# Kernel optimization log

Hardware: AMD Instinct MI355X
Metric: run time of the kernel (lower is better)

Reference implementation:

```python
import jax, jax.numpy as jnp
import numpy as np

C64 = jnp.complex64


def _ry(t):  # scalar angle -> [2,2] complex
    c = jnp.cos(t / 2).astype(C64)
    s = jnp.sin(t / 2).astype(C64)
    return jnp.stack([jnp.stack([c, -s]), jnp.stack([s, c])])


def _rz(t):  # scalar angle -> [2,2] complex (diagonal)
    p = jnp.exp(-0.5j * t.astype(C64))
    z = jnp.zeros((), C64)
    return jnp.stack([jnp.stack([p, z]), jnp.stack([z, jnp.conj(p)])])


def _rx_batch(t):  # t: [B] -> [B,2,2] complex (per-sample RX encoding gate)
    c = jnp.cos(t / 2).astype(C64)
    s = jnp.sin(t / 2).astype(C64)
    row0 = jnp.stack([c, -1j * s], axis=-1)
    row1 = jnp.stack([-1j * s, c], axis=-1)
    return jnp.stack([row0, row1], axis=-2)


def _apply_1q(state, gate, wire, n):
    # state: [B, 2^n]; wire 0 is the most significant bit (PennyLane convention)
    B = state.shape[0]
    pre, post = 2 ** wire, 2 ** (n - wire - 1)
    s = state.reshape(B, pre, 2, post)
    if gate.ndim == 2:
        s = jnp.einsum('ij,bpjq->bpiq', gate, s)
    else:  # per-sample gate [B,2,2]
        s = jnp.einsum('bij,bpjq->bpiq', gate, s)
    return s.reshape(B, -1)


def _apply_cnot(state, wire, n):
    # CNOT with control=wire, target=wire+1 (adjacent wires)
    B = state.shape[0]
    pre, post = 2 ** wire, 2 ** (n - wire - 2)
    s = state.reshape(B, pre, 2, 2, post)
    # control==1 block gets its target axis flipped
    s = jnp.concatenate([s[:, :, :1], s[:, :, 1:, ::-1]], axis=2)
    return s.reshape(B, -1)


def _circuit(x, params):
    # Batched statevector simulation of: RX(x_i) encoding, then n_layers of
    # (RY,RZ,RY) per wire + CNOT chain, then <Z_i> per wire.
    B, n = x.shape
    L = params.shape[0]
    state = jnp.zeros((B, 2 ** n), C64).at[:, 0].set(1.0)
    for i in range(n):
        state = _apply_1q(state, _rx_batch(x[:, i]), i, n)
    for l in range(L):
        for i in range(n):
            # RY(p0) first, then RZ(p1), then RY(p2): fuse into one 2x2 gate
            g = _ry(params[l, i, 2]) @ _rz(params[l, i, 1]) @ _ry(params[l, i, 0])
            state = _apply_1q(state, g, i, n)
        for i in range(n - 1):
            state = _apply_cnot(state, i, n)
    probs = jnp.abs(state) ** 2  # [B, 2^n] float32
    ez = []
    for i in range(n):
        p = probs.reshape(B, 2 ** i, 2, 2 ** (n - i - 1))
        ez.append(p[:, :, 0].sum((1, 2)) - p[:, :, 1].sum((1, 2)))
    return jnp.stack(ez, axis=1)  # [B, n]


def setup_inputs() -> dict:
    key = jax.random.key(0)
    k1, k2, k3, _ = jax.random.split(key, 4)
    B, n, L = 8192, 12, 3
    return {
        'x': jax.random.normal(k1, (B, n), jnp.float32),
        'params': jax.random.normal(k2, (L, n, 3), jnp.float32),
        'head_w': jax.random.normal(k3, (1, n), jnp.float32) / np.float32(np.sqrt(n)),
        'head_b': jnp.zeros((1,), jnp.float32),
    }


def reference(x, params, head_w, head_b):
    ez = _circuit(x, params)           # [B, n] per-wire Z expectations
    out = ez @ head_w.T + head_b       # Linear(n, 1)
    return out[:, 0]                   # squeeze(-1) -> [B]
```

## Files before the change

kernel.cpp:

```cpp
#include <hip/hip_runtime.h>
#include <math.h>

#define NQ 12
#define NTH 256
#define NL 3
#define GRID 768

typedef _Float16 h8 __attribute__((ext_vector_type(8)));
typedef _Float16 h4 __attribute__((ext_vector_type(4)));
typedef _Float16 hf2 __attribute__((ext_vector_type(2)));
typedef float f4 __attribute__((ext_vector_type(4)));

#define MFMA __builtin_amdgcn_mfma_f32_16x16x32_f16


__device__ __forceinline__ int sfx(int v) {
    v ^= v >> 1; v ^= v >> 2; v ^= v >> 4; v ^= v >> 8;
    return v;
}
__device__ __forceinline__ int swzf(int off) {
    return off ^ (((((off >> 6) ^ (off >> 9)) & 7)) << 3);
}
__device__ __forceinline__ int swz1(int off) {
    return off ^ ((((off >> 5) ^ (off >> 9)) & 7) << 3);
}
__device__ __forceinline__ int swzw(int off) {
    return off ^ (((off >> 6) & 7) << 3);
}

__device__ __forceinline__ unsigned pk2(float lo, float hi) {
    hf2 t_; t_.x = (_Float16)lo; t_.y = (_Float16)hi;
    unsigned r_; __builtin_memcpy(&r_, &t_, 4); return r_;
}

__device__ __forceinline__ h8 xition(f4 re, f4 im) {
    unsigned a0 = pk2(re.x, re.y), a1 = pk2(re.z, re.w);
    unsigned b0 = pk2(im.x, im.y), b1 = pk2(im.z, im.w);
    asm("v_permlane32_swap_b32 %0, %1" : "+v"(a0), "+v"(b0));
    asm("v_permlane16_swap_b32 %0, %1" : "+v"(a0), "+v"(b0));
    asm("v_permlane32_swap_b32 %0, %1" : "+v"(a1), "+v"(b1));
    asm("v_permlane16_swap_b32 %0, %1" : "+v"(a1), "+v"(b1));
    union { unsigned u[4]; h8 v; } r_;
    r_.u[0] = a0; r_.u[1] = a1; r_.u[2] = b0; r_.u[3] = b1;
    return r_.v;
}

__global__ void __launch_bounds__(NTH, 3)
qsim_kernel(const float* __restrict__ x,
            const float* __restrict__ params,
            const float* __restrict__ head_w,
            const float* __restrict__ head_b,
            float* __restrict__ out, int Btot) {
    __shared__ __align__(16) _Float16 Sst[16384];
    __shared__ __align__(16) _Float16 Wl[6144];
    __shared__ float wlo[64], whi[64];
    __shared__ float csx[6 * 24], snx[6 * 24];
    __shared__ float Gs0[96];
    __shared__ __align__(16) float fct[2][48][2];
    __shared__ float wred[8];
    float* Gs = (float*)Sst;

    const int t = threadIdx.x, blk = blockIdx.x;
    const int npairs = (Btot + 1) >> 1;

    if (t < 36) {
        float p0 = params[t * 3 + 0], p1 = params[t * 3 + 1], p2 = params[t * 3 + 2];
        float c0 = cosf(0.5f * p0), s0 = sinf(0.5f * p0);
        float ch = cosf(0.5f * p1), sh = sinf(0.5f * p1);
        float c2 = cosf(0.5f * p2), s2 = sinf(0.5f * p2);
        float pr_ = ch, pi = -sh, qr = ch, qi = sh;
        float A = c2 * c0, Bc = s2 * s0, Cc = c2 * s0, D = s2 * c0;
        float* g = &Gs[t * 8];
        g[0] = A * pr_ - Bc * qr;  g[1] = A * pi - Bc * qi;
        g[2] = -Cc * pr_ - D * qr; g[3] = -Cc * pi - D * qi;
        g[4] = D * pr_ + Cc * qr;  g[5] = D * pi + Cc * qi;
        g[6] = -Bc * pr_ + A * qr; g[7] = -Bc * pi + A * qi;
    }
    if (t >= 36 && t < 180) {
        int idx = t - 36;
        int pr = idx / 24, w = idx - pr * 24;
        int pairIdx = blk + pr * GRID;
        if (pairIdx < npairs) {
            int smp = pairIdx * 2 + (w >= 12 ? 1 : 0);
            int wire = (w >= 12) ? (w - 12) : w;
            if (smp < Btot) {
                float xv = 0.5f * x[smp * NQ + wire];
                csx[pr * 24 + w] = cosf(xv);
                snx[pr * 24 + w] = sinf(xv);
            }
        }
    }
    if (t >= 192) {
        int v = t - 192; float s = 0.f, s2 = 0.f;
#pragma unroll
        for (int be = 0; be < 6; ++be) {
            s  += ((v >> be) & 1) ? -head_w[11 - be] : head_w[11 - be];
            s2 += ((v >> be) & 1) ? -head_w[5 - be]  : head_w[5 - be];
        }
        wlo[v] = s; whi[v] = s2;
    }
    __syncthreads();

    if (t < 96) Gs0[t] = Gs[t];
#pragma unroll
    for (int i = 0; i < 24; ++i) {
        int e = i * 256 + t;
        int s = (e >> 10) + 3;
        int idx = e & 1023;
        int n = idx >> 5, k = idx & 31;
        int rp = n >> 4, tp = n & 15, rr = k >> 4, tt = k & 31 & 15;
        int l = s / 3, g = s - 3 * l;
        float ur = 1.f, ui = 0.f;
#pragma unroll
        for (int jj = 0; jj < 4; ++jj) {
            int wire = 11 - (4 * g + jj);
            const float* gp = &Gs[(l * 12 + wire) * 8];
            int rb = (tp >> jj) & 1, cb = (tt >> jj) & 1;
            float gr = gp[(rb * 2 + cb) * 2], gi = gp[(rb * 2 + cb) * 2 + 1];
            float nr = ur * gr - ui * gi;
            float ni = ur * gi + ui * gr;
            ur = nr; ui = ni;
        }
        float val = (rp == 0) ? ((rr == 0) ? ur : -ui)
                              : ((rr == 0) ? ui : ur);
        Wl[swzw(e)] = (_Float16)val;
    }
    __syncthreads();

    const int wv = t >> 6, u = t & 15, q = (t >> 4) & 3;
    const int wbs = swzw(u * 32 + q * 8);
    int g0b[4], g1b[4];
#pragma unroll
    for (int mb = 0; mb < 4; ++mb) {
        int m_ = wv * 64 + (u >> 2) * 16 + mb * 4 + (u & 3);
        g0b[mb] = swzf(m_ * 32 + q * 8);
        int l_ = t & 63;
        int m1 = ((l_ >> 2) & 3) * 64 + (l_ & 3) * 16 + wv * 4 + mb;
        g1b[mb] = swz1(m1 * 32 + q * 8);
    }
    const int sb = (t * 32) ^ (((t ^ (t >> 4)) & 7) << 3);

    const int s4 = (u ^ (u >> 1) ^ (u >> 2) ^ (u >> 3)) & 15;
    const int P4 = s4 & 1, q0 = q & 1, q1 = q >> 1;
    const int j7 = q1 ^ P4, j6 = q0 ^ q1 ^ P4;
    const int wv0 = wv & 1, wv1 = wv >> 1;
    int Eo[4], PwR[4];
#pragma unroll
    for (int r = 0; r < 4; ++r) {
        int r0 = r & 1, r1 = r >> 1;
        int j5 = r1 ^ j6, j4 = (r0 ^ r1) ^ j6;
        int j3 = wv1 ^ j4, j2 = wv0 ^ wv1 ^ j4;
        int m0 = s4 * 16 + j7 * 8 + j6 * 4 + j5 * 2 + j4;
        Eo[r]  = swzf(m0 * 32 + j3 * 8 + j2 * 4);
        PwR[r] = (wv0 ^ wv1 ^ j4);
    }
    const int Pw0 = wv0 ^ wv1 ^ j6;
    const int wloB = j6 * 48 + (wv1 ^ j6) * 8 + (wv0 ^ wv1 ^ j6) * 4 + Pw0 * 3;
    const float whiv = whi[s4 * 4 + j7 * 2 + j6];
    const f4 Z = {0.f, 0.f, 0.f, 0.f};

    const int iu = (t ^ (t >> 1)) & 0xFF;
    const int aI = iu >> 4;
    const int bI = 16 + (iu & 15);
    const int flip = (t & 1) << 3;

#define ST16(off_, va_, vb_) { h8 w_;                                        \
    w_[0] = (_Float16)(va_).x; w_[1] = (_Float16)(va_).y;                    \
    w_[2] = (_Float16)(va_).z; w_[3] = (_Float16)(va_).w;                    \
    w_[4] = (_Float16)(vb_).x; w_[5] = (_Float16)(vb_).y;                    \
    w_[6] = (_Float16)(vb_).z; w_[7] = (_Float16)(vb_).w;                    \
    *(h8*)&Sst[off_] = w_; }

#define PST1(CMP_, r_) {                                                     \
    bool pw_ = PwR[r_] != 0;                                                 \
    { float v0=eRA[0].CMP_, v1=eRA[1].CMP_, v2=eRA[2].CMP_, v3=eRA[3].CMP_;  \
      h4 w_; w_.x=(_Float16)(pw_?v2:v0); w_.y=(_Float16)(pw_?v3:v1);         \
             w_.z=(_Float16)(pw_?v1:v3); w_.w=(_Float16)(pw_?v0:v2);         \
      *(h4*)&Sst[Eo[r_]] = w_; }                                             \
    { float v0=eIA[0].CMP_, v1=eIA[1].CMP_, v2=eIA[2].CMP_, v3=eIA[3].CMP_;  \
      h4 w_; w_.x=(_Float16)(pw_?v2:v0); w_.y=(_Float16)(pw_?v3:v1);         \
             w_.z=(_Float16)(pw_?v1:v3); w_.w=(_Float16)(pw_?v0:v2);         \
      *(h4*)&Sst[Eo[r_] ^ 16] = w_; }                                        \
    { float v0=eRB[0].CMP_, v1=eRB[1].CMP_, v2=eRB[2].CMP_, v3=eRB[3].CMP_;  \
      h4 w_; w_.x=(_Float16)(pw_?v2:v0); w_.y=(_Float16)(pw_?v3:v1);         \
             w_.z=(_Float16)(pw_?v1:v3); w_.w=(_Float16)(pw_?v0:v2);         \
      *(h4*)&Sst[Eo[r_] + 8192] = w_; }                                      \
    { float v0=eIB[0].CMP_, v1=eIB[1].CMP_, v2=eIB[2].CMP_, v3=eIB[3].CMP_;  \
      h4 w_; w_.x=(_Float16)(pw_?v2:v0); w_.y=(_Float16)(pw_?v3:v1);         \
             w_.z=(_Float16)(pw_?v1:v3); w_.w=(_Float16)(pw_?v0:v2);         \
      *(h4*)&Sst[(Eo[r_] ^ 16) + 8192] = w_; } }

#define RD1(CMP_, dr_) {                                                     \
    int b_ = wloB ^ (dr_);                                                   \
    float w0_ = whiv + wlo[b_],     w1_ = whiv + wlo[b_ ^ 1];                \
    float w2_ = whiv + wlo[b_ ^ 3], w3_ = whiv + wlo[b_ ^ 2];                \
    racc0 = fmaf(fmaf(eRA[0].CMP_, eRA[0].CMP_, eIA[0].CMP_*eIA[0].CMP_), w0_, racc0); \
    racc0 = fmaf(fmaf(eRA[1].CMP_, eRA[1].CMP_, eIA[1].CMP_*eIA[1].CMP_), w1_, racc0); \
    racc0 = fmaf(fmaf(eRA[2].CMP_, eRA[2].CMP_, eIA[2].CMP_*eIA[2].CMP_), w2_, racc0); \
    racc0 = fmaf(fmaf(eRA[3].CMP_, eRA[3].CMP_, eIA[3].CMP_*eIA[3].CMP_), w3_, racc0); \
    racc1 = fmaf(fmaf(eRB[0].CMP_, eRB[0].CMP_, eIB[0].CMP_*eIB[0].CMP_), w0_, racc1); \
    racc1 = fmaf(fmaf(eRB[1].CMP_, eRB[1].CMP_, eIB[1].CMP_*eIB[1].CMP_), w1_, racc1); \
    racc1 = fmaf(fmaf(eRB[2].CMP_, eRB[2].CMP_, eIB[2].CMP_*eIB[2].CMP_), w2_, racc1); \
    racc1 = fmaf(fmaf(eRB[3].CMP_, eRB[3].CMP_, eIB[3].CMP_*eIB[3].CMP_), w3_, racc1); }

#pragma unroll 1
    for (int pr = 0; ; ++pr) {
        const int pairIdx = blk + pr * GRID;
        if (pairIdx >= npairs) break;

        if (t < 96) {
            int s_ = t / 48, k_ = t - s_ * 48;
            int grp = k_ >> 4, h = k_ & 15;
            int wbase = (grp == 0) ? 3 : (grp == 1) ? 7 : 11;
            const float* cs_ = &csx[pr * 24 + s_ * 12];
            const float* sn_ = &snx[pr * 24 + s_ * 12];
            float ur = 1.f, ui = 0.f;
#pragma unroll
            for (int jj = 0; jj < 4; ++jj) {
                int w = wbase - jj;
                int bit = (h >> jj) & 1;
                const float* g = &Gs0[w * 8];
                float c = cs_[w], sn = sn_[w];
                float tr, ti;
                if (bit == 0) { tr = g[0] * c + g[3] * sn; ti = g[1] * c - g[2] * sn; }
                else          { tr = g[4] * c + g[7] * sn; ti = g[5] * c - g[6] * sn; }
                float nr = ur * tr - ui * ti, ni = ur * ti + ui * tr;
                ur = nr; ui = ni;
            }
            fct[s_][k_][0] = ur; fct[s_][k_][1] = ui;
        }
        __syncthreads();

#pragma unroll
        for (int s_ = 0; s_ < 2; ++s_) {
            const int SOFF = s_ * 8192;
            float ar = fct[s_][aI][0], ai = fct[s_][aI][1];
            float br = fct[s_][bI][0], bi = fct[s_][bI][1];
            float abr = ar * br - ai * bi, abi = ar * bi + ai * br;
            float cr[16], ci[16];
#pragma unroll
            for (int k = 0; k < 16; ++k) {
                cr[k] = fct[s_][32 + (k ^ flip)][0];
                ci[k] = fct[s_][32 + (k ^ flip)][1];
            }
            h8 wr0, wr1, wi0, wi1;
#pragma unroll
            for (int tau = 0; tau < 16; ++tau) {
                const int cidx = tau ^ (tau >> 1);
                float vr = abr * cr[cidx] - abi * ci[cidx];
                float vi = abr * ci[cidx] + abi * cr[cidx];
                if (tau < 8) { wr0[tau] = (_Float16)vr; wi0[tau] = (_Float16)vi; }
                else         { wr1[tau - 8] = (_Float16)vr; wi1[tau - 8] = (_Float16)vi; }
            }
            const int off0 = t * 32;
            *(h8*)&Sst[swzf(off0)      + SOFF] = wr0;
            *(h8*)&Sst[swzf(off0 + 8)  + SOFF] = wr1;
            *(h8*)&Sst[swzf(off0 + 16) + SOFF] = wi0;
            *(h8*)&Sst[swzf(off0 + 24) + SOFF] = wi1;
        }
        __syncthreads();

        float racc0 = 0.f, racc1 = 0.f;
#pragma unroll
        for (int l = 1; l < NL; ++l) {
            {
                const int sW = ((l - 1) * 3 + 0) * 1024;
                h8 bf0 = *(const h8*)&Wl[sW + wbs];
                h8 bf1 = *(const h8*)&Wl[sW + 512 + wbs];
                h8 aA[4], aB[4];
#pragma unroll
                for (int mb = 0; mb < 4; ++mb) {
                    aA[mb] = *(const h8*)&Sst[g0b[mb]];
                    aB[mb] = *(const h8*)&Sst[g0b[mb] + 8192];
                }
                __syncthreads();
                f4 cR[4], cI[4];
#pragma unroll
                for (int mb = 0; mb < 4; ++mb) {
                    cR[mb] = MFMA(aA[mb], bf0, Z, 0, 0, 0);
                    cI[mb] = MFMA(aA[mb], bf1, Z, 0, 0, 0);
                }
                ST16(sb,        cR[0], cR[1]) ST16(sb ^ 8,  cR[2], cR[3])
                ST16(sb ^ 16,   cI[0], cI[1]) ST16(sb ^ 24, cI[2], cI[3])
#pragma unroll
                for (int mb = 0; mb < 4; ++mb) {
                    cR[mb] = MFMA(aB[mb], bf0, Z, 0, 0, 0);
                    cI[mb] = MFMA(aB[mb], bf1, Z, 0, 0, 0);
                }
                ST16(sb + 8192,        cR[0], cR[1]) ST16((sb ^ 8) + 8192,  cR[2], cR[3])
                ST16((sb ^ 16) + 8192, cI[0], cI[1]) ST16((sb ^ 24) + 8192, cI[2], cI[3])
                __syncthreads();
            }
            {
                const int sW1 = ((l - 1) * 3 + 1) * 1024, sW2 = ((l - 1) * 3 + 2) * 1024;
                h8 bg0 = *(const h8*)&Wl[sW1 + wbs];
                h8 bg1 = *(const h8*)&Wl[sW1 + 512 + wbs];
                h8 bh0 = *(const h8*)&Wl[sW2 + wbs];
                h8 bh1 = *(const h8*)&Wl[sW2 + 512 + wbs];
                h8 gA[4], gB[4];
#pragma unroll
                for (int mb = 0; mb < 4; ++mb) {
                    gA[mb] = *(const h8*)&Sst[g1b[mb]];
                    gB[mb] = *(const h8*)&Sst[g1b[mb] + 8192];
                }
                if (l < NL - 1) __syncthreads();
                f4 eRA[4], eIA[4], eRB[4], eIB[4];
                {
                    f4 dR[4], dI[4]; h8 t2[4];
#pragma unroll
                    for (int mb = 0; mb < 4; ++mb) {
                        dR[mb] = MFMA(gA[mb], bg0, Z, 0, 0, 0);
                        dI[mb] = MFMA(gA[mb], bg1, Z, 0, 0, 0);
                    }
#pragma unroll
                    for (int mb = 0; mb < 4; ++mb) t2[mb] = xition(dR[mb], dI[mb]);
#pragma unroll
                    for (int mb = 0; mb < 4; ++mb) {
                        eRA[mb] = MFMA(t2[mb], bh0, Z, 0, 0, 0);
                        eIA[mb] = MFMA(t2[mb], bh1, Z, 0, 0, 0);
                    }
                }
                {
                    f4 dR[4], dI[4]; h8 t2[4];
#pragma unroll
                    for (int mb = 0; mb < 4; ++mb) {
                        dR[mb] = MFMA(gB[mb], bg0, Z, 0, 0, 0);
                        dI[mb] = MFMA(gB[mb], bg1, Z, 0, 0, 0);
                    }
#pragma unroll
                    for (int mb = 0; mb < 4; ++mb) t2[mb] = xition(dR[mb], dI[mb]);
#pragma unroll
                    for (int mb = 0; mb < 4; ++mb) {
                        eRB[mb] = MFMA(t2[mb], bh0, Z, 0, 0, 0);
                        eIB[mb] = MFMA(t2[mb], bh1, Z, 0, 0, 0);
                    }
                }
                if (l < NL - 1) {
                    PST1(x, 0) PST1(y, 1) PST1(z, 2) PST1(w, 3)
                    __syncthreads();
                } else {
                    RD1(x, 0) RD1(y, 31) RD1(z, 63) RD1(w, 32)
                }
            }
        }
#pragma unroll
        for (int o = 32; o >= 1; o >>= 1) {
            racc0 += __shfl_xor(racc0, o, 64);
            racc1 += __shfl_xor(racc1, o, 64);
        }
        if ((t & 63) == 0) { wred[wv] = racc0; wred[4 + wv] = racc1; }
        __syncthreads();
        if (t < 2) {
            int smp = pairIdx * 2 + t;
            if (smp < Btot) {
                float r = head_b[0];
#pragma unroll
                for (int i2 = 0; i2 < 4; ++i2) r += wred[t * 4 + i2];
                out[smp] = r;
            }
        }
    }
}

extern "C" void kernel_launch(void* const* d_in, const int* in_sizes, int n_in,
                              void* d_out, int out_size, void* d_ws, size_t ws_size,
                              hipStream_t stream) {
    const float* x = (const float*)d_in[0];
    const float* params = (const float*)d_in[1];
    const float* head_w = (const float*)d_in[2];
    const float* head_b = (const float*)d_in[3];
    float* out = (float*)d_out;
    int B = in_sizes[0] / NQ;

    hipLaunchKernelGGL(qsim_kernel, dim3(GRID), dim3(NTH), 0, stream,
                       x, params, head_w, head_b, out, B);
}
```

Measured before the change: 104.6 us.

## Hoist weight fragments into registers, prefetch next factors, drop redundant barriers

Loads all twelve MFMA B-operand fragments from LDS into registers once before the pair loop instead of reloading them every layer. Builds the next pair's per-sample factor table at the end of the current iteration so it shares the existing reduction barrier. Removes two __syncthreads per iteration, and reads factor pairs as float4 vectors. Register pressure goes up, and barrier removal depends on buffer reuse staying race-free.

```diff
diff --git a/kernel.cpp b/kernel.cpp
--- a/kernel.cpp
+++ b/kernel.cpp
@@ -108,7 +108,7 @@
         int s = (e >> 10) + 3;
         int idx = e & 1023;
         int n = idx >> 5, k = idx & 31;
-        int rp = n >> 4, tp = n & 15, rr = k >> 4, tt = k & 31 & 15;
+        int rp = n >> 4, tp = n & 15, rr = k >> 4, tt = k & 15;
         int l = s / 3, g = s - 3 * l;
         float ur = 1.f, ui = 0.f;
 #pragma unroll
@@ -129,6 +129,17 @@
 
     const int wv = t >> 6, u = t & 15, q = (t >> 4) & 3;
     const int wbs = swzw(u * 32 + q * 8);
+
+    h8 Wb[12];
+#pragma unroll
+    for (int l = 0; l < 2; ++l)
+#pragma unroll
+        for (int g = 0; g < 3; ++g) {
+            const int sW = (l * 3 + g) * 1024;
+            Wb[l * 6 + g * 2]     = *(const h8*)&Wl[sW + wbs];
+            Wb[l * 6 + g * 2 + 1] = *(const h8*)&Wl[sW + 512 + wbs];
+        }
+
     int g0b[4], g1b[4];
 #pragma unroll
     for (int mb = 0; mb < 4; ++mb) {
@@ -163,6 +174,30 @@
     const int aI = iu >> 4;
     const int bI = 16 + (iu & 15);
     const int flip = (t & 1) << 3;
+
+    auto build_fct = [&](int pr_) {
+        if (t < 96 && blk + pr_ * GRID < npairs) {
+            int s_ = t / 48, k_ = t - s_ * 48;
+            int grp = k_ >> 4, h = k_ & 15;
+            int wbase = (grp == 0) ? 3 : (grp == 1) ? 7 : 11;
+            const float* cs_ = &csx[pr_ * 24 + s_ * 12];
+            const float* sn_ = &snx[pr_ * 24 + s_ * 12];
+            float ur = 1.f, ui = 0.f;
+#pragma unroll
+            for (int jj = 0; jj < 4; ++jj) {
+                int w = wbase - jj;
+                int bit = (h >> jj) & 1;
+                const float* g = &Gs0[w * 8];
+                float c = cs_[w], sn = sn_[w];
+                float tr, ti;
+                if (bit == 0) { tr = g[0] * c + g[3] * sn; ti = g[1] * c - g[2] * sn; }
+                else          { tr = g[4] * c + g[7] * sn; ti = g[5] * c - g[6] * sn; }
+                float nr = ur * tr - ui * ti, ni = ur * ti + ui * tr;
+                ur = nr; ui = ni;
+            }
+            fct[s_][k_][0] = ur; fct[s_][k_][1] = ui;
+        }
+    };
 
 #define ST16(off_, va_, vb_) { h8 w_;                                        \
     w_[0] = (_Float16)(va_).x; w_[1] = (_Float16)(va_).y;                    \
@@ -203,33 +238,13 @@
     racc1 = fmaf(fmaf(eRB[2].CMP_, eRB[2].CMP_, eIB[2].CMP_*eIB[2].CMP_), w2_, racc1); \
     racc1 = fmaf(fmaf(eRB[3].CMP_, eRB[3].CMP_, eIB[3].CMP_*eIB[3].CMP_), w3_, racc1); }
 
+    build_fct(0);
+    __syncthreads();
+
 #pragma unroll 1
     for (int pr = 0; ; ++pr) {
         const int pairIdx = blk + pr * GRID;
         if (pairIdx >= npairs) break;
-
-        if (t < 96) {
-            int s_ = t / 48, k_ = t - s_ * 48;
-            int grp = k_ >> 4, h = k_ & 15;
-            int wbase = (grp == 0) ? 3 : (grp == 1) ? 7 : 11;
-            const float* cs_ = &csx[pr * 24 + s_ * 12];
-            const float* sn_ = &snx[pr * 24 + s_ * 12];
-            float ur = 1.f, ui = 0.f;
-#pragma unroll
-            for (int jj = 0; jj < 4; ++jj) {
-                int w = wbase - jj;
-                int bit = (h >> jj) & 1;
-                const float* g = &Gs0[w * 8];
-                float c = cs_[w], sn = sn_[w];
-                float tr, ti;
-                if (bit == 0) { tr = g[0] * c + g[3] * sn; ti = g[1] * c - g[2] * sn; }
-                else          { tr = g[4] * c + g[7] * sn; ti = g[5] * c - g[6] * sn; }
-                float nr = ur * tr - ui * ti, ni = ur * ti + ui * tr;
-                ur = nr; ui = ni;
-            }
-            fct[s_][k_][0] = ur; fct[s_][k_][1] = ui;
-        }
-        __syncthreads();
 
 #pragma unroll
         for (int s_ = 0; s_ < 2; ++s_) {
@@ -239,9 +254,9 @@
             float abr = ar * br - ai * bi, abi = ar * bi + ai * br;
             float cr[16], ci[16];
 #pragma unroll
-            for (int k = 0; k < 16; ++k) {
-                cr[k] = fct[s_][32 + (k ^ flip)][0];
-                ci[k] = fct[s_][32 + (k ^ flip)][1];
+            for (int k2 = 0; k2 < 16; k2 += 2) {
+                f4 v = *(const f4*)&fct[s_][32 + (k2 ^ flip)][0];
+                cr[k2] = v.x; ci[k2] = v.y; cr[k2 + 1] = v.z; ci[k2 + 1] = v.w;
             }
             h8 wr0, wr1, wi0, wi1;
 #pragma unroll
@@ -258,22 +273,19 @@
             *(h8*)&Sst[swzf(off0 + 16) + SOFF] = wi0;
             *(h8*)&Sst[swzf(off0 + 24) + SOFF] = wi1;
         }
-        __syncthreads();
 
         float racc0 = 0.f, racc1 = 0.f;
 #pragma unroll
         for (int l = 1; l < NL; ++l) {
             {
-                const int sW = ((l - 1) * 3 + 0) * 1024;
-                h8 bf0 = *(const h8*)&Wl[sW + wbs];
-                h8 bf1 = *(const h8*)&Wl[sW + 512 + wbs];
+                const h8 bf0 = Wb[(l - 1) * 6 + 0];
+                const h8 bf1 = Wb[(l - 1) * 6 + 1];
                 h8 aA[4], aB[4];
 #pragma unroll
                 for (int mb = 0; mb < 4; ++mb) {
                     aA[mb] = *(const h8*)&Sst[g0b[mb]];
                     aB[mb] = *(const h8*)&Sst[g0b[mb] + 8192];
                 }
-                __syncthreads();
                 f4 cR[4], cI[4];
 #pragma unroll
                 for (int mb = 0; mb < 4; ++mb) {
@@ -292,11 +304,10 @@
                 __syncthreads();
             }
             {
-                const int sW1 = ((l - 1) * 3 + 1) * 1024, sW2 = ((l - 1) * 3 + 2) * 1024;
-                h8 bg0 = *(const h8*)&Wl[sW1 + wbs];
-                h8 bg1 = *(const h8*)&Wl[sW1 + 512 + wbs];
-                h8 bh0 = *(const h8*)&Wl[sW2 + wbs];
-                h8 bh1 = *(const h8*)&Wl[sW2 + 512 + wbs];
+                const h8 bg0 = Wb[(l - 1) * 6 + 2];
+                const h8 bg1 = Wb[(l - 1) * 6 + 3];
+                const h8 bh0 = Wb[(l - 1) * 6 + 4];
+                const h8 bh1 = Wb[(l - 1) * 6 + 5];
                 h8 gA[4], gB[4];
 #pragma unroll
                 for (int mb = 0; mb < 4; ++mb) {
@@ -343,6 +354,7 @@
                 }
             }
         }
+        build_fct(pr + 1);
 #pragma unroll
         for (int o = 32; o >= 1; o >>= 1) {
             racc0 += __shfl_xor(racc0, o, 64);
```

Result: slower. 124.9 us (+19.4%).

## Prebuild next pair's factor table and drop wave-local barriers around state staging

Applied to the files above, without the earlier changes.

Factor-table construction for the next sample pair now happens at the end of the current iteration, so it is covered by the existing reduction barrier instead of needing its own. Two __syncthreads are removed: one after the initial state store and one between the A-operand loads and the in-place MFMA result stores. This relies on each wave reading only LDS regions it wrote itself. The 16-entry coefficient reads are also vectorised into float4 LDS loads. If any cross-wave LDS dependency exists, dropping those barriers risks races.

```diff
diff --git a/kernel.cpp b/kernel.cpp
--- a/kernel.cpp
+++ b/kernel.cpp
@@ -108,7 +108,7 @@
         int s = (e >> 10) + 3;
         int idx = e & 1023;
         int n = idx >> 5, k = idx & 31;
-        int rp = n >> 4, tp = n & 15, rr = k >> 4, tt = k & 31 & 15;
+        int rp = n >> 4, tp = n & 15, rr = k >> 4, tt = k & 15;
         int l = s / 3, g = s - 3 * l;
         float ur = 1.f, ui = 0.f;
 #pragma unroll
@@ -163,6 +163,28 @@
     const int aI = iu >> 4;
     const int bI = 16 + (iu & 15);
     const int flip = (t & 1) << 3;
+
+#define BUILD_FCT(pr_) {                                                     \
+    if (t < 96 && blk + (pr_) * GRID < npairs) {                             \
+        int s_ = t / 48, k_ = t - s_ * 48;                                   \
+        int grp = k_ >> 4, h = k_ & 15;                                      \
+        int wbase = (grp == 0) ? 3 : (grp == 1) ? 7 : 11;                    \
+        const float* cs_ = &csx[(pr_) * 24 + s_ * 12];                       \
+        const float* sn_ = &snx[(pr_) * 24 + s_ * 12];                       \
+        float ur = 1.f, ui = 0.f;                                            \
+        _Pragma("unroll") for (int jj = 0; jj < 4; ++jj) {                   \
+            int w = wbase - jj;                                              \
+            int bit = (h >> jj) & 1;                                         \
+            const float* g = &Gs0[w * 8];                                    \
+            float c = cs_[w], sn = sn_[w];                                   \
+            float tr, ti;                                                    \
+            if (bit == 0) { tr = g[0] * c + g[3] * sn; ti = g[1] * c - g[2] * sn; } \
+            else          { tr = g[4] * c + g[7] * sn; ti = g[5] * c - g[6] * sn; } \
+            float nr = ur * tr - ui * ti, ni = ur * ti + ui * tr;            \
+            ur = nr; ui = ni;                                                \
+        }                                                                    \
+        fct[s_][k_][0] = ur; fct[s_][k_][1] = ui;                            \
+    } }
 
 #define ST16(off_, va_, vb_) { h8 w_;                                        \
     w_[0] = (_Float16)(va_).x; w_[1] = (_Float16)(va_).y;                    \
@@ -203,33 +225,13 @@
     racc1 = fmaf(fmaf(eRB[2].CMP_, eRB[2].CMP_, eIB[2].CMP_*eIB[2].CMP_), w2_, racc1); \
     racc1 = fmaf(fmaf(eRB[3].CMP_, eRB[3].CMP_, eIB[3].CMP_*eIB[3].CMP_), w3_, racc1); }
 
+    BUILD_FCT(0)
+    __syncthreads();
+
 #pragma unroll 1
     for (int pr = 0; ; ++pr) {
         const int pairIdx = blk + pr * GRID;
         if (pairIdx >= npairs) break;
-
-        if (t < 96) {
-            int s_ = t / 48, k_ = t - s_ * 48;
-            int grp = k_ >> 4, h = k_ & 15;
-            int wbase = (grp == 0) ? 3 : (grp == 1) ? 7 : 11;
-            const float* cs_ = &csx[pr * 24 + s_ * 12];
-            const float* sn_ = &snx[pr * 24 + s_ * 12];
-            float ur = 1.f, ui = 0.f;
-#pragma unroll
-            for (int jj = 0; jj < 4; ++jj) {
-                int w = wbase - jj;
-                int bit = (h >> jj) & 1;
-                const float* g = &Gs0[w * 8];
-                float c = cs_[w], sn = sn_[w];
-                float tr, ti;
-                if (bit == 0) { tr = g[0] * c + g[3] * sn; ti = g[1] * c - g[2] * sn; }
-                else          { tr = g[4] * c + g[7] * sn; ti = g[5] * c - g[6] * sn; }
-                float nr = ur * tr - ui * ti, ni = ur * ti + ui * tr;
-                ur = nr; ui = ni;
-            }
-            fct[s_][k_][0] = ur; fct[s_][k_][1] = ui;
-        }
-        __syncthreads();
 
 #pragma unroll
         for (int s_ = 0; s_ < 2; ++s_) {
@@ -239,9 +241,9 @@
             float abr = ar * br - ai * bi, abi = ar * bi + ai * br;
             float cr[16], ci[16];
 #pragma unroll
-            for (int k = 0; k < 16; ++k) {
-                cr[k] = fct[s_][32 + (k ^ flip)][0];
-                ci[k] = fct[s_][32 + (k ^ flip)][1];
+            for (int k2 = 0; k2 < 16; k2 += 2) {
+                f4 v = *(const f4*)&fct[s_][32 + (k2 ^ flip)][0];
+                cr[k2] = v.x; ci[k2] = v.y; cr[k2 + 1] = v.z; ci[k2 + 1] = v.w;
             }
             h8 wr0, wr1, wi0, wi1;
 #pragma unroll
@@ -258,7 +260,6 @@
             *(h8*)&Sst[swzf(off0 + 16) + SOFF] = wi0;
             *(h8*)&Sst[swzf(off0 + 24) + SOFF] = wi1;
         }
-        __syncthreads();
 
         float racc0 = 0.f, racc1 = 0.f;
 #pragma unroll
@@ -273,7 +274,6 @@
                     aA[mb] = *(const h8*)&Sst[g0b[mb]];
                     aB[mb] = *(const h8*)&Sst[g0b[mb] + 8192];
                 }
-                __syncthreads();
                 f4 cR[4], cI[4];
 #pragma unroll
                 for (int mb = 0; mb < 4; ++mb) {
@@ -343,6 +343,7 @@
                 }
             }
         }
+        BUILD_FCT(pr + 1)
 #pragma unroll
         for (int o = 32; o >= 1; o >>= 1) {
             racc0 += __shfl_xor(racc0, o, 64);
```

After: 107.7 us. 2.9% more time.
